# Kernel tuning notes

Measured on AMD Instinct MI355X. Metric: run time of the kernel, lower is better.

The kernel has to match this reference:

```python
import jax, jax.numpy as jnp
import numpy as np

N_TRIALS, T, INPUT_DIM = 32, 512, 64
N, R, OUTPUT_DIM = 4096, 8, 64
DT = 0.1


def setup_inputs() -> dict:
    key = jax.random.key(0)
    k_inp, k_B, k_W, k_m, k_n = jax.random.split(key, 5)
    inp = jax.random.normal(k_inp, (N_TRIALS, T, INPUT_DIM), dtype=jnp.float32)
    B = jax.random.normal(k_B, (N, INPUT_DIM), dtype=jnp.float32)
    W = jax.random.normal(k_W, (OUTPUT_DIM, N), dtype=jnp.float32) / np.sqrt(N)
    m = jax.random.normal(k_m, (N, R), dtype=jnp.float32)
    n = jax.random.normal(k_n, (N, R), dtype=jnp.float32)
    return {"inp": inp, "B": B, "W": W, "m": m, "n": n}


def reference(inp, B, W, m, n):
    # inp: [b, t, i]; B: [N, i]; W: [o, N]; m, n: [N, r]
    n_trials = inp.shape[0]
    # Precompute input projection for all steps: [t, b, N]
    inp_proj = jnp.einsum('bti,ni->tbn', inp, B)

    def step(x, u):
        # x: [b, N] voltage; u: [b, N] projected input at this step
        # sigmoid(x) @ (m n^T / N)^T == ((sigmoid(x) @ n) @ m^T) / N
        rec = (jax.nn.sigmoid(x) @ n) @ m.T / N
        x_new = (1.0 - DT) * x + DT * (rec + u)
        y = jax.nn.sigmoid(x_new) @ W.T  # [b, o]
        return x_new, (x_new, y)

    x0 = jnp.zeros((n_trials, N), dtype=inp.dtype)
    _, (xs, ys) = jax.lax.scan(step, x0, inp_proj)
    # xs: [t, b, N]; ys: [t, b, o]
    x_seq = jnp.concatenate([x0[None], xs], axis=0).transpose(1, 0, 2)  # [b, t+1, N]
    output_seq = ys.transpose(1, 0, 2)  # [b, t, o]
    return (x_seq, output_seq)
```

## Files before the change

### kernel.cpp

```cpp
#include <hip/hip_runtime.h>

static constexpr int BTRIALS = 32;
static constexpr int TSTEPS  = 512;
static constexpr int IDIM    = 64;
static constexpr int NDIM    = 4096;
static constexpr int RDIM    = 8;
static constexpr int ODIM    = 64;

__device__ __forceinline__ float fast_sigmoid(float x) {
    float e = __builtin_amdgcn_exp2f(x * -1.44269504088896340736f);
    return __builtin_amdgcn_rcpf(1.0f + e);
}

template <int CTRL, int RMASK>
__device__ __forceinline__ float dpp_add(float v) {
    int moved = __builtin_amdgcn_update_dpp(0, __float_as_int(v), CTRL, RMASK, 0xf, true);
    return v + __int_as_float(moved);
}

__device__ __forceinline__ float wave_reduce_to_lane63(float v) {
    v = dpp_add<0x111, 0xf>(v);
    v = dpp_add<0x112, 0xf>(v);
    v = dpp_add<0x114, 0xf>(v);
    v = dpp_add<0x118, 0xf>(v);
    v = dpp_add<0x142, 0xa>(v);
    v = dpp_add<0x143, 0xc>(v);
    return v;
}

__global__ __launch_bounds__(256) void pre_gemm(const float* __restrict__ inp,
                                                const float* __restrict__ Bm,
                                                float* __restrict__ u,
                                                int t0, int rows) {
    __shared__ __align__(16) float At[64][68];
    __shared__ __align__(16) float Bt[64][68];
    const int tid = threadIdx.x;
    const int c4  = (tid & 15) * 4;
    const int rq  = tid >> 4;
    const int mbase = blockIdx.x * 64;
    const int nbase = blockIdx.y * 64;

    #pragma unroll
    for (int rr = 0; rr < 4; ++rr) {
        const int rloc = rr * 16 + rq;
        const int mr = mbase + rloc;
        float4 a = make_float4(0.f, 0.f, 0.f, 0.f);
        if (mr < rows) {
            const int b  = mr & 31;
            const int tl = mr >> 5;
            a = *(const float4*)(inp + ((size_t)b * TSTEPS + (t0 + tl)) * IDIM + c4);
        }
        At[c4 + 0][rloc] = a.x; At[c4 + 1][rloc] = a.y;
        At[c4 + 2][rloc] = a.z; At[c4 + 3][rloc] = a.w;
        const int n = nbase + rloc;
        float4 bb = *(const float4*)(Bm + (size_t)n * IDIM + c4);
        Bt[c4 + 0][rloc] = bb.x; Bt[c4 + 1][rloc] = bb.y;
        Bt[c4 + 2][rloc] = bb.z; Bt[c4 + 3][rloc] = bb.w;
    }
    __syncthreads();

    const int m4 = (tid >> 4) * 4;
    const int n4 = (tid & 15) * 4;
    float acc[4][4];
    #pragma unroll
    for (int i = 0; i < 4; ++i)
        #pragma unroll
        for (int j = 0; j < 4; ++j) acc[i][j] = 0.f;

    #pragma unroll 8
    for (int k = 0; k < 64; ++k) {
        float4 a = *(const float4*)&At[k][m4];
        float4 w = *(const float4*)&Bt[k][n4];
        float av[4] = {a.x, a.y, a.z, a.w};
        float wv[4] = {w.x, w.y, w.z, w.w};
        #pragma unroll
        for (int i = 0; i < 4; ++i)
            #pragma unroll
            for (int j = 0; j < 4; ++j)
                acc[i][j] = fmaf(av[i], wv[j], acc[i][j]);
    }

    #pragma unroll
    for (int i = 0; i < 4; ++i) {
        const int mr = mbase + m4 + i;
        if (mr < rows) {
            float4 o = make_float4(acc[i][0] * 0.1f, acc[i][1] * 0.1f,
                                   acc[i][2] * 0.1f, acc[i][3] * 0.1f);
            *(float4*)(u + (size_t)mr * NDIM + nbase + n4) = o;
        }
    }
}

__global__ __launch_bounds__(512, 2) void scan_kernel(const float* __restrict__ mmat,
                                                      const float* __restrict__ nmat,
                                                      const float* __restrict__ u,
                                                      float* __restrict__ xseq,
                                                      float* __restrict__ xstate,
                                                      int t0, int tc) {
    const int b    = blockIdx.x;
    const int tid  = threadIdx.x;
    const int j0   = tid * 8;
    const int lane = tid & 63;
    const int wv   = tid >> 6;

    __shared__ __align__(16) float wlds[64];
    __shared__ __align__(16) float projb[8];

    float nm[8][8], mmr[8][8], x[8];
    const float4* np4 = (const float4*)(nmat + (size_t)j0 * RDIM);
    const float4* mp4 = (const float4*)(mmat + (size_t)j0 * RDIM);
    const float mscale = 0.1f / 4096.0f;
    #pragma unroll
    for (int j = 0; j < 8; ++j) {
        float4 a = np4[j * 2], c = np4[j * 2 + 1];
        nm[j][0] = a.x; nm[j][1] = a.y; nm[j][2] = a.z; nm[j][3] = a.w;
        nm[j][4] = c.x; nm[j][5] = c.y; nm[j][6] = c.z; nm[j][7] = c.w;
        float4 d = mp4[j * 2], e = mp4[j * 2 + 1];
        mmr[j][0] = d.x * mscale; mmr[j][1] = d.y * mscale;
        mmr[j][2] = d.z * mscale; mmr[j][3] = d.w * mscale;
        mmr[j][4] = e.x * mscale; mmr[j][5] = e.y * mscale;
        mmr[j][6] = e.z * mscale; mmr[j][7] = e.w * mscale;
    }

    if (t0 == 0) {
        #pragma unroll
        for (int j = 0; j < 8; ++j) x[j] = 0.0f;
        float* z = xseq + (size_t)b * (TSTEPS + 1) * NDIM + j0;
        *(float4*)(z + 0) = make_float4(0.f, 0.f, 0.f, 0.f);
        *(float4*)(z + 4) = make_float4(0.f, 0.f, 0.f, 0.f);
    } else {
        const float* xs = xstate + (size_t)b * NDIM + j0;
        float4 v0 = *(const float4*)(xs + 0);
        float4 v1 = *(const float4*)(xs + 4);
        x[0] = v0.x; x[1] = v0.y; x[2] = v0.z; x[3] = v0.w;
        x[4] = v1.x; x[5] = v1.y; x[6] = v1.z; x[7] = v1.w;
    }

    float uv[8];
    {
        const float* up = u + ((size_t)0 * BTRIALS + b) * NDIM + j0;
        float4 v0 = *(const float4*)(up + 0);
        float4 v1 = *(const float4*)(up + 4);
        uv[0] = v0.x; uv[1] = v0.y; uv[2] = v0.z; uv[3] = v0.w;
        uv[4] = v1.x; uv[5] = v1.y; uv[6] = v1.z; uv[7] = v1.w;
    }

    for (int tl = 0; tl < tc; ++tl) {
        const int tn = (tl + 1 < tc) ? (tl + 1) : tl;
        const float* upn = u + ((size_t)tn * BTRIALS + b) * NDIM + j0;
        float4 pf0 = *(const float4*)(upn + 0);
        float4 pf1 = *(const float4*)(upn + 4);

        float part[8];
        #pragma unroll
        for (int r = 0; r < 8; ++r) part[r] = 0.0f;
        #pragma unroll
        for (int j = 0; j < 8; ++j) {
            float s = fast_sigmoid(x[j]);
            #pragma unroll
            for (int r = 0; r < 8; ++r) part[r] = fmaf(s, nm[j][r], part[r]);
        }

        #pragma unroll
        for (int r = 0; r < 8; ++r) part[r] = wave_reduce_to_lane63(part[r]);

        if (lane == 63) {
            *(float4*)&wlds[wv * 8 + 0] = make_float4(part[0], part[1], part[2], part[3]);
            *(float4*)&wlds[wv * 8 + 4] = make_float4(part[4], part[5], part[6], part[7]);
        }
        __syncthreads();
        if (tid < 64) {
            float v = wlds[tid];
            v += __shfl_xor(v, 8);
            v += __shfl_xor(v, 16);
            v += __shfl_xor(v, 32);
            if (tid < 8) projb[tid] = v;
        }
        __syncthreads();

        float4 p0 = *(const float4*)&projb[0];
        float4 p1 = *(const float4*)&projb[4];
        float proj[8] = {p0.x, p0.y, p0.z, p0.w, p1.x, p1.y, p1.z, p1.w};

        float* xrow = xseq + ((size_t)b * (TSTEPS + 1) + (t0 + tl + 1)) * NDIM + j0;
        #pragma unroll
        for (int j = 0; j < 8; ++j) {
            float rec = proj[0] * mmr[j][0];
            #pragma unroll
            for (int r = 1; r < 8; ++r) rec = fmaf(proj[r], mmr[j][r], rec);
            x[j] = fmaf(0.9f, x[j], rec + uv[j]);
        }
        *(float4*)(xrow + 0) = make_float4(x[0], x[1], x[2], x[3]);
        *(float4*)(xrow + 4) = make_float4(x[4], x[5], x[6], x[7]);

        uv[0] = pf0.x; uv[1] = pf0.y; uv[2] = pf0.z; uv[3] = pf0.w;
        uv[4] = pf1.x; uv[5] = pf1.y; uv[6] = pf1.z; uv[7] = pf1.w;
    }

    float* xs = xstate + (size_t)b * NDIM + j0;
    *(float4*)(xs + 0) = make_float4(x[0], x[1], x[2], x[3]);
    *(float4*)(xs + 4) = make_float4(x[4], x[5], x[6], x[7]);
}

__global__ __launch_bounds__(256) void y_gemm(const float* __restrict__ xseq,
                                              const float* __restrict__ Wm,
                                              float* __restrict__ yout) {
    __shared__ __align__(16) float Sg[64][68];
    __shared__ __align__(16) float Wt[64][68];
    const int tid = threadIdx.x;
    const int c4  = (tid & 15) * 4;
    const int rq  = tid >> 4;
    const int mbase = blockIdx.x * 64;
    const int m4 = (tid >> 4) * 4;
    const int o4 = (tid & 15) * 4;

    float acc[4][4];
    #pragma unroll
    for (int i = 0; i < 4; ++i)
        #pragma unroll
        for (int j = 0; j < 4; ++j) acc[i][j] = 0.f;

    for (int kc = 0; kc < NDIM; kc += 64) {
        __syncthreads();
        #pragma unroll
        for (int rr = 0; rr < 4; ++rr) {
            const int rloc = rr * 16 + rq;
            const int m = mbase + rloc;
            const int brow = m >> 9;
            float4 a = *(const float4*)(xseq + (size_t)(m + brow + 1) * NDIM + kc + c4);
            Sg[c4 + 0][rloc] = fast_sigmoid(a.x);
            Sg[c4 + 1][rloc] = fast_sigmoid(a.y);
            Sg[c4 + 2][rloc] = fast_sigmoid(a.z);
            Sg[c4 + 3][rloc] = fast_sigmoid(a.w);
            float4 w = *(const float4*)(Wm + (size_t)rloc * NDIM + kc + c4);
            Wt[c4 + 0][rloc] = w.x; Wt[c4 + 1][rloc] = w.y;
            Wt[c4 + 2][rloc] = w.z; Wt[c4 + 3][rloc] = w.w;
        }
        __syncthreads();
        #pragma unroll 8
        for (int k = 0; k < 64; ++k) {
            float4 a = *(const float4*)&Sg[k][m4];
            float4 w = *(const float4*)&Wt[k][o4];
            float av[4] = {a.x, a.y, a.z, a.w};
            float wv[4] = {w.x, w.y, w.z, w.w};
            #pragma unroll
            for (int i = 0; i < 4; ++i)
                #pragma unroll
                for (int j = 0; j < 4; ++j)
                    acc[i][j] = fmaf(av[i], wv[j], acc[i][j]);
        }
    }

    #pragma unroll
    for (int i = 0; i < 4; ++i) {
        *(float4*)(yout + (size_t)(mbase + m4 + i) * ODIM + o4) =
            make_float4(acc[i][0], acc[i][1], acc[i][2], acc[i][3]);
    }
}

extern "C" void kernel_launch(void* const* d_in, const int* in_sizes, int n_in,
                              void* d_out, int out_size, void* d_ws, size_t ws_size,
                              hipStream_t stream) {
    const float* inp = (const float*)d_in[0];
    const float* Bm  = (const float*)d_in[1];
    const float* Wm  = (const float*)d_in[2];
    const float* mm  = (const float*)d_in[3];
    const float* nm  = (const float*)d_in[4];

    float* out  = (float*)d_out;
    float* xseq = out;
    float* yout = out + (size_t)BTRIALS * (TSTEPS + 1) * NDIM;

    float* xstate = (float*)d_ws;
    float* ubuf   = xstate + (size_t)BTRIALS * NDIM;

    const size_t xbytes  = (size_t)BTRIALS * NDIM * sizeof(float);
    const size_t perstep = (size_t)BTRIALS * NDIM * sizeof(float);
    size_t avail = (ws_size > xbytes) ? (ws_size - xbytes) : 0;
    int Tc = (int)(avail / perstep);
    if (Tc > TSTEPS) Tc = TSTEPS;
    if (Tc < 1) Tc = 1;

    for (int t0 = 0; t0 < TSTEPS; t0 += Tc) {
        const int tc = (TSTEPS - t0 < Tc) ? (TSTEPS - t0) : Tc;
        const int rows = tc * BTRIALS;
        dim3 g1((rows + 63) / 64, NDIM / 64);
        pre_gemm<<<g1, 256, 0, stream>>>(inp, Bm, ubuf, t0, rows);
        scan_kernel<<<BTRIALS, 512, 0, stream>>>(mm, nm, ubuf, xseq, xstate, t0, tc);
    }
    y_gemm<<<(BTRIALS * TSTEPS) / 64, 256, 0, stream>>>(xseq, Wm, yout);
}
```

Baseline: 1.146 ms.

## Use bf16 MFMA for output GEMM and remove a barrier from scan

The output projection kernel now runs on bf16 MFMA 16x16x32 instructions. It converts sigmoid activations and W to bf16 in registers instead of doing an LDS-tiled fp32 FMA GEMM. Separately, the scan step double-buffers its LDS partials and finishes the cross-wave reduction with DPP plus readlane in every wave, which removes one __syncthreads per timestep and the projb broadcast. The decay-plus-input term is computed before the barrier so it overlaps the wait. Bf16 rounding lowers the output precision, and the GEMM reads global memory directly without LDS reuse.

```diff
diff --git a/kernel.cpp b/kernel.cpp
--- a/kernel.cpp
+++ b/kernel.cpp
@@ -26,6 +26,12 @@
     v = dpp_add<0x142, 0xa>(v);
     v = dpp_add<0x143, 0xc>(v);
     return v;
+}
+
+__device__ __forceinline__ short f2bf(float f) {
+    unsigned u = __float_as_uint(f);
+    u += 0x7FFFu + ((u >> 16) & 1u);
+    return (short)(u >> 16);
 }
 
 __global__ __launch_bounds__(256) void pre_gemm(const float* __restrict__ inp,
@@ -103,8 +109,7 @@
     const int lane = tid & 63;
     const int wv   = tid >> 6;
 
-    __shared__ __align__(16) float wlds[64];
-    __shared__ __align__(16) float projb[8];
+    __shared__ __align__(16) float wlds[2][64];
 
     float nm[8][8], mmr[8][8], x[8];
     const float4* np4 = (const float4*)(nmat + (size_t)j0 * RDIM);
@@ -146,6 +151,7 @@
     }
 
     for (int tl = 0; tl < tc; ++tl) {
+        const int buf = tl & 1;
         const int tn = (tl + 1 < tc) ? (tl + 1) : tl;
         const float* upn = u + ((size_t)tn * BTRIALS + b) * NDIM + j0;
         float4 pf0 = *(const float4*)(upn + 0);
@@ -160,35 +166,37 @@
             #pragma unroll
             for (int r = 0; r < 8; ++r) part[r] = fmaf(s, nm[j][r], part[r]);
         }
-
         #pragma unroll
         for (int r = 0; r < 8; ++r) part[r] = wave_reduce_to_lane63(part[r]);
 
         if (lane == 63) {
-            *(float4*)&wlds[wv * 8 + 0] = make_float4(part[0], part[1], part[2], part[3]);
-            *(float4*)&wlds[wv * 8 + 4] = make_float4(part[4], part[5], part[6], part[7]);
-        }
+            #pragma unroll
+            for (int r = 0; r < 8; ++r) wlds[buf][r * 8 + wv] = part[r];
+        }
+
+        float xd[8];
+        #pragma unroll
+        for (int j = 0; j < 8; ++j) xd[j] = fmaf(0.9f, x[j], uv[j]);
+
         __syncthreads();
-        if (tid < 64) {
-            float v = wlds[tid];
-            v += __shfl_xor(v, 8);
-            v += __shfl_xor(v, 16);
-            v += __shfl_xor(v, 32);
-            if (tid < 8) projb[tid] = v;
-        }
-        __syncthreads();
-
-        float4 p0 = *(const float4*)&projb[0];
-        float4 p1 = *(const float4*)&projb[4];
-        float proj[8] = {p0.x, p0.y, p0.z, p0.w, p1.x, p1.y, p1.z, p1.w};
+
+        float v = wlds[buf][lane];
+        v = dpp_add<0x111, 0xf>(v);
+        v = dpp_add<0x112, 0xf>(v);
+        v = dpp_add<0x114, 0xf>(v);
+
+        float ps[8];
+        #pragma unroll
+        for (int r = 0; r < 8; ++r)
+            ps[r] = __int_as_float(__builtin_amdgcn_readlane(__float_as_int(v), r * 8 + 7));
 
         float* xrow = xseq + ((size_t)b * (TSTEPS + 1) + (t0 + tl + 1)) * NDIM + j0;
         #pragma unroll
         for (int j = 0; j < 8; ++j) {
-            float rec = proj[0] * mmr[j][0];
-            #pragma unroll
-            for (int r = 1; r < 8; ++r) rec = fmaf(proj[r], mmr[j][r], rec);
-            x[j] = fmaf(0.9f, x[j], rec + uv[j]);
+            float acc = xd[j];
+            #pragma unroll
+            for (int r = 0; r < 8; ++r) acc = fmaf(ps[r], mmr[j][r], acc);
+            x[j] = acc;
         }
         *(float4*)(xrow + 0) = make_float4(x[0], x[1], x[2], x[3]);
         *(float4*)(xrow + 4) = make_float4(x[4], x[5], x[6], x[7]);
@@ -202,59 +210,56 @@
     *(float4*)(xs + 4) = make_float4(x[4], x[5], x[6], x[7]);
 }
 
+typedef short v8s __attribute__((ext_vector_type(8)));
+typedef float v4f __attribute__((ext_vector_type(4)));
+
 __global__ __launch_bounds__(256) void y_gemm(const float* __restrict__ xseq,
                                               const float* __restrict__ Wm,
                                               float* __restrict__ yout) {
-    __shared__ __align__(16) float Sg[64][68];
-    __shared__ __align__(16) float Wt[64][68];
-    const int tid = threadIdx.x;
-    const int c4  = (tid & 15) * 4;
-    const int rq  = tid >> 4;
-    const int mbase = blockIdx.x * 64;
-    const int m4 = (tid >> 4) * 4;
-    const int o4 = (tid & 15) * 4;
-
-    float acc[4][4];
-    #pragma unroll
-    for (int i = 0; i < 4; ++i)
-        #pragma unroll
-        for (int j = 0; j < 4; ++j) acc[i][j] = 0.f;
-
-    for (int kc = 0; kc < NDIM; kc += 64) {
-        __syncthreads();
-        #pragma unroll
-        for (int rr = 0; rr < 4; ++rr) {
-            const int rloc = rr * 16 + rq;
-            const int m = mbase + rloc;
-            const int brow = m >> 9;
-            float4 a = *(const float4*)(xseq + (size_t)(m + brow + 1) * NDIM + kc + c4);
-            Sg[c4 + 0][rloc] = fast_sigmoid(a.x);
-            Sg[c4 + 1][rloc] = fast_sigmoid(a.y);
-            Sg[c4 + 2][rloc] = fast_sigmoid(a.z);
-            Sg[c4 + 3][rloc] = fast_sigmoid(a.w);
-            float4 w = *(const float4*)(Wm + (size_t)rloc * NDIM + kc + c4);
-            Wt[c4 + 0][rloc] = w.x; Wt[c4 + 1][rloc] = w.y;
-            Wt[c4 + 2][rloc] = w.z; Wt[c4 + 3][rloc] = w.w;
-        }
-        __syncthreads();
-        #pragma unroll 8
-        for (int k = 0; k < 64; ++k) {
-            float4 a = *(const float4*)&Sg[k][m4];
-            float4 w = *(const float4*)&Wt[k][o4];
-            float av[4] = {a.x, a.y, a.z, a.w};
-            float wv[4] = {w.x, w.y, w.z, w.w};
-            #pragma unroll
-            for (int i = 0; i < 4; ++i)
-                #pragma unroll
-                for (int j = 0; j < 4; ++j)
-                    acc[i][j] = fmaf(av[i], wv[j], acc[i][j]);
-        }
-    }
-
-    #pragma unroll
-    for (int i = 0; i < 4; ++i) {
-        *(float4*)(yout + (size_t)(mbase + m4 + i) * ODIM + o4) =
-            make_float4(acc[i][0], acc[i][1], acc[i][2], acc[i][3]);
+    const int tid  = threadIdx.x;
+    const int lane = tid & 63;
+    const int mt   = blockIdx.x * 4 + (tid >> 6);
+    const int lm   = lane & 15;
+    const int kq   = lane >> 4;
+
+    const int m = mt * 16 + lm;
+    const int g = m + (m >> 9) + 1;
+    const float* pa = xseq + (size_t)g * NDIM + kq * 8;
+    const float* pw = Wm + (size_t)lm * NDIM + kq * 8;
+
+    v4f acc[4];
+    #pragma unroll
+    for (int ot = 0; ot < 4; ++ot) acc[ot] = (v4f){0.f, 0.f, 0.f, 0.f};
+
+    for (int kc = 0; kc < NDIM; kc += 32) {
+        float4 a0 = *(const float4*)(pa + kc);
+        float4 a1 = *(const float4*)(pa + kc + 4);
+        v8s af;
+        af[0] = f2bf(fast_sigmoid(a0.x)); af[1] = f2bf(fast_sigmoid(a0.y));
+        af[2] = f2bf(fast_sigmoid(a0.z)); af[3] = f2bf(fast_sigmoid(a0.w));
+        af[4] = f2bf(fast_sigmoid(a1.x)); af[5] = f2bf(fast_sigmoid(a1.y));
+        af[6] = f2bf(fast_sigmoid(a1.z)); af[7] = f2bf(fast_sigmoid(a1.w));
+        #pragma unroll
+        for (int ot = 0; ot < 4; ++ot) {
+            const float* pwo = pw + (size_t)ot * 16 * NDIM + kc;
+            float4 w0 = *(const float4*)(pwo);
+            float4 w1 = *(const float4*)(pwo + 4);
+            v8s bf;
+            bf[0] = f2bf(w0.x); bf[1] = f2bf(w0.y);
+            bf[2] = f2bf(w0.z); bf[3] = f2bf(w0.w);
+            bf[4] = f2bf(w1.x); bf[5] = f2bf(w1.y);
+            bf[6] = f2bf(w1.z); bf[7] = f2bf(w1.w);
+            acc[ot] = __builtin_amdgcn_mfma_f32_16x16x32_bf16(af, bf, acc[ot], 0, 0, 0);
+        }
+    }
+
+    #pragma unroll
+    for (int ot = 0; ot < 4; ++ot) {
+        #pragma unroll
+        for (int r = 0; r < 4; ++r) {
+            const int row = mt * 16 + kq * 4 + r;
+            yout[(size_t)row * ODIM + ot * 16 + lm] = acc[ot][r];
+        }
     }
 }
 
```

After: 1.062 ms. 7.3% less time.
